# Performance work log

Measured on AMD Instinct MI355X. Metric: run time of the kernel, lower is better.

Reference implementation:

```python
import jax, jax.numpy as jnp
import numpy as np

N = 100_000      # nodes
F_IN = 512       # input feature dim
HID = 8          # hidden per head (layer 1)
HEADS = 8        # heads layer 1
CLS = 7          # num classes (layer 2 out, 1 head)
E = 1_600_000    # random edges (self-loops added in reference)
NEG_SLOPE = 0.2  # PyG GATConv default leaky_relu slope


def setup_inputs() -> dict:
    key = jax.random.key(0)
    ks = jax.random.split(key, 10)
    s1 = 1.0 / np.sqrt(F_IN)
    s2 = 1.0 / np.sqrt(HID * HEADS)
    return {
        "x": jax.random.normal(ks[0], (N, F_IN), jnp.float32),
        "edge_index": jax.random.randint(ks[1], (2, E), 0, N, dtype=jnp.int32),
        "W1": jax.random.normal(ks[2], (F_IN, HEADS * HID), jnp.float32) * s1,
        "a_src1": jax.random.normal(ks[3], (HEADS, HID), jnp.float32) * s1,
        "a_dst1": jax.random.normal(ks[4], (HEADS, HID), jnp.float32) * s1,
        "b1": jnp.zeros((HEADS * HID,), jnp.float32),
        "W2": jax.random.normal(ks[5], (HEADS * HID, CLS), jnp.float32) * s2,
        "a_src2": jax.random.normal(ks[6], (1, CLS), jnp.float32) * s2,
        "a_dst2": jax.random.normal(ks[7], (1, CLS), jnp.float32) * s2,
        "b2": jnp.zeros((CLS,), jnp.float32),
    }


def gat_layer(x, edge_index, W, a_src, a_dst, bias, concat):
    """PyG GATConv (eval mode): linear -> per-edge LeakyReLU score -> edge-softmax over
    incoming edges per dst node -> weighted scatter-sum of src messages."""
    n = x.shape[0]
    H, C = a_src.shape
    h = (x @ W).reshape(n, H, C)                      # [N, H, C]
    src, dst = edge_index[0], edge_index[1]
    alpha_src = (h * a_src).sum(-1)                   # [N, H]
    alpha_dst = (h * a_dst).sum(-1)                   # [N, H]
    e = jax.nn.leaky_relu(alpha_src[src] + alpha_dst[dst], NEG_SLOPE)  # [E, H]
    # numerically stable segment softmax over edges grouped by dst
    m = jax.ops.segment_max(e, dst, num_segments=n)   # [N, H]
    p = jnp.exp(e - m[dst])                           # [E, H]
    denom = jax.ops.segment_sum(p, dst, num_segments=n)
    alpha = p / denom[dst]                            # [E, H]
    out = jax.ops.segment_sum(alpha[:, :, None] * h[src], dst, num_segments=n)  # [N, H, C]
    out = out.reshape(n, H * C) if concat else out.mean(axis=1)
    return out + bias


def reference(x, edge_index, W1, a_src1, a_dst1, b1, W2, a_src2, a_dst2, b2):
    # add self-loops (GATConv default add_self_loops=True)
    loops = jnp.arange(N, dtype=edge_index.dtype)
    ei = jnp.concatenate([edge_index, jnp.stack([loops, loops])], axis=1)
    h = jax.nn.elu(gat_layer(x, ei, W1, a_src1, a_dst1, b1, concat=True))
    out = gat_layer(h, ei, W2, a_src2, a_dst2, b2, concat=False)
    return jax.nn.log_softmax(out, axis=1)
```

## Files before the change

kernel.cpp:

```cpp
#include <hip/hip_runtime.h>
#include <hip/hip_bf16.h>

#define NEG_SLOPE 0.2f
#define SB 256
#define HWG 384

typedef __attribute__((ext_vector_type(8))) short bfrag;
typedef __attribute__((ext_vector_type(4))) float f32x4;
typedef unsigned short ushort_t;

__device__ __forceinline__ float lrelu(float x) {
    return x >= 0.0f ? x : NEG_SLOPE * x;
}
__device__ __forceinline__ unsigned short f2bf(float f) {
    unsigned int u = __float_as_uint(f);
    u += 0x7fffu + ((u >> 16) & 1u);
    return (unsigned short)(u >> 16);
}
__device__ __forceinline__ float bf2f(unsigned short h) {
    return __uint_as_float(((unsigned int)h) << 16);
}
__device__ __forceinline__ float u2lo(unsigned int u) {
    return __uint_as_float(u << 16);
}
__device__ __forceinline__ float u2hi(unsigned int u) {
    return __uint_as_float(u & 0xffff0000u);
}

__global__ __launch_bounds__(256) void hist_prep_kernel(
    const int* __restrict__ edst, int* __restrict__ bcnt, int E, int NB,
    const float* __restrict__ W1, ushort_t* __restrict__ Whi,
    ushort_t* __restrict__ Wlo) {
    if (blockIdx.x < 128) {
        int t = blockIdx.x * 256 + threadIdx.x;
        int k = t >> 6, c = t & 63;
        float w = W1[t];
        unsigned short hi = f2bf(w);
        float rem = w - bf2f(hi);
        int dst = (k >> 7) * 8192 + c * 128 + (k & 127);
        Whi[dst] = hi;
        Wlo[dst] = f2bf(rem);
        return;
    }
    __shared__ int hist[512];
    int tid = threadIdx.x;
    for (int i = tid; i < NB; i += 256) hist[i] = 0;
    __syncthreads();
    int wg = blockIdx.x - 128;
    int CH = (E + HWG - 1) / HWG;
    int st = wg * CH, en = min(st + CH, E);
    for (int i = st + tid; i < en; i += 256)
        atomicAdd(&hist[edst[i] >> 8], 1);
    __syncthreads();
    for (int i = tid; i < NB; i += 256)
        if (hist[i] > 0) atomicAdd(&bcnt[i], hist[i]);
}

__global__ __launch_bounds__(512) void bscan_kernel(
    const int* __restrict__ bcnt, int* __restrict__ boff, int* __restrict__ bcur,
    int* __restrict__ csr_off, int NB, int N, int E) {
    __shared__ int s[512];
    int t = threadIdx.x;
    int v = (t < NB) ? bcnt[t] : 0;
    s[t] = v;
    __syncthreads();
    for (int off = 1; off < 512; off <<= 1) {
        int tv = (t >= off) ? s[t - off] : 0;
        __syncthreads();
        s[t] += tv;
        __syncthreads();
    }
    if (t < NB) {
        int o = s[t] - v;
        boff[t] = o;
        bcur[t] = o;
    }
    if (t == 0) {
        boff[NB] = E;
        csr_off[N] = E;
    }
}

__global__ __launch_bounds__(256) void gemm_bscatter_kernel(
    const float* __restrict__ x, const ushort_t* __restrict__ Whi,
    const ushort_t* __restrict__ Wlo, ushort_t* __restrict__ h1b, int n,
    const int* __restrict__ esrc, const int* __restrict__ edst,
    int* __restrict__ bcur, int2* __restrict__ ebuf, int E, int NB,
    const float* __restrict__ a_src1, const float* __restrict__ a_dst1,
    float* __restrict__ as1, float* __restrict__ ad1) {
    __shared__ int sbuf[1536];
    const int tid = threadIdx.x;

    if (blockIdx.x < SB) {
        int* hist = sbuf;
        int* base = sbuf + 512;
        int* rank = sbuf + 1024;
        for (int i = tid; i < NB; i += 256) { hist[i] = 0; rank[i] = 0; }
        __syncthreads();
        int CH = (E + SB - 1) / SB;
        int st = blockIdx.x * CH, en = min(st + CH, E);
        for (int i = st + tid; i < en; i += 256)
            atomicAdd(&hist[edst[i] >> 8], 1);
        __syncthreads();
        for (int b = tid; b < NB; b += 256)
            if (hist[b] > 0) base[b] = atomicAdd(&bcur[b], hist[b]);
        __syncthreads();
        for (int i = st + tid; i < en; i += 256) {
            int d = edst[i], s = esrc[i];
            int b = d >> 8;
            int r = atomicAdd(&rank[b], 1);
            ebuf[base[b] + r] = make_int2(s, d);
        }
        return;
    }

    const int lane = tid & 63;
    const int wave = tid >> 6;
    const int l15 = lane & 15;
    const int lq = lane >> 4;
    const int wb = (blockIdx.x - SB) * 64 + wave * 16;

    f32x4 acc[4];
    #pragma unroll
    for (int t = 0; t < 4; t++) acc[t] = (f32x4){0.f, 0.f, 0.f, 0.f};

    const int arow = min(wb + l15, n - 1);
    const float* xr = x + (size_t)arow * 512;

    for (int p = 0; p < 4; p++) {
        const ushort_t* whp = Whi + p * 8192;
        const ushort_t* wlp = Wlo + p * 8192;
        #pragma unroll
        for (int step = 0; step < 4; step++) {
            int kloc = step * 32 + lq * 8;
            int kb = p * 128 + kloc;
            float4 v0 = *(const float4*)&xr[kb];
            float4 v1 = *(const float4*)&xr[kb + 4];
            float xf[8] = {v0.x, v0.y, v0.z, v0.w, v1.x, v1.y, v1.z, v1.w};
            bfrag ah, al;
            #pragma unroll
            for (int j = 0; j < 8; j++) {
                unsigned short hi = f2bf(xf[j]);
                float rem = xf[j] - bf2f(hi);
                ah[j] = (short)hi;
                al[j] = (short)f2bf(rem);
            }
            #pragma unroll
            for (int t = 0; t < 4; t++) {
                int nrow = t * 16 + l15;
                bfrag bh = *(const bfrag*)&whp[nrow * 128 + kloc];
                bfrag bl = *(const bfrag*)&wlp[nrow * 128 + kloc];
                acc[t] = __builtin_amdgcn_mfma_f32_16x16x32_bf16(al, bh, acc[t], 0, 0, 0);
                acc[t] = __builtin_amdgcn_mfma_f32_16x16x32_bf16(ah, bl, acc[t], 0, 0, 0);
                acc[t] = __builtin_amdgcn_mfma_f32_16x16x32_bf16(ah, bh, acc[t], 0, 0, 0);
            }
        }
    }
    #pragma unroll
    for (int t = 0; t < 4; t++) {
        #pragma unroll
        for (int reg = 0; reg < 4; reg++) {
            int grow = wb + lq * 4 + reg;
            if (grow < n) h1b[(size_t)grow * 64 + t * 16 + l15] = f2bf(acc[t][reg]);
        }
    }
    const int j7 = l15 & 7;
    const int wrow = wb + lq * 4 + (j7 & 3);
    #pragma unroll
    for (int t = 0; t < 4; t++) {
        int cidx = t * 16 + l15;
        float cs = a_src1[cidx];
        float cd = a_dst1[cidx];
        float ps0 = acc[t][0] * cs, ps1 = acc[t][1] * cs;
        float ps2 = acc[t][2] * cs, ps3 = acc[t][3] * cs;
        float pd0 = acc[t][0] * cd, pd1 = acc[t][1] * cd;
        float pd2 = acc[t][2] * cd, pd3 = acc[t][3] * cd;
        #pragma unroll
        for (int off = 1; off < 8; off <<= 1) {
            ps0 += __shfl_xor(ps0, off);
            ps1 += __shfl_xor(ps1, off);
            ps2 += __shfl_xor(ps2, off);
            ps3 += __shfl_xor(ps3, off);
            pd0 += __shfl_xor(pd0, off);
            pd1 += __shfl_xor(pd1, off);
            pd2 += __shfl_xor(pd2, off);
            pd3 += __shfl_xor(pd3, off);
        }
        int h = (t << 1) | (l15 >> 3);
        if (wrow < n) {
            if (j7 < 4) {
                float sv = j7 == 0 ? ps0 : j7 == 1 ? ps1 : j7 == 2 ? ps2 : ps3;
                as1[wrow * 8 + h] = sv;
            } else {
                float dv = j7 == 4 ? pd0 : j7 == 5 ? pd1 : j7 == 6 ? pd2 : pd3;
                ad1[wrow * 8 + h] = dv;
            }
        }
    }
}

__global__ __launch_bounds__(256) void finalize_kernel(
    const int* __restrict__ boff, const int2* __restrict__ ebuf,
    int* __restrict__ csr_off, int* __restrict__ col, int N, int NB) {
    int tid = threadIdx.x;
    int b = blockIdx.x;
    __shared__ int cnt[256];
    __shared__ int cur[256];
    __shared__ int sc[256];
    cnt[tid] = 0;
    __syncthreads();
    int st = boff[b], en = boff[b + 1];
    for (int i = st + tid; i < en; i += 256)
        atomicAdd(&cnt[ebuf[i].y & 255], 1);
    __syncthreads();
    int v = cnt[tid];
    sc[tid] = v;
    __syncthreads();
    for (int off = 1; off < 256; off <<= 1) {
        int tv = (tid >= off) ? sc[tid - off] : 0;
        __syncthreads();
        sc[tid] += tv;
        __syncthreads();
    }
    int dbase = b << 8;
    int nd = min(256, N - dbase);
    int o = st + sc[tid] - v;
    if (tid < nd) {
        csr_off[dbase + tid] = o;
        cur[tid] = o;
    }
    __syncthreads();
    for (int i = st + tid; i < en; i += 256) {
        int2 p = ebuf[i];
        int r = atomicAdd(&cur[p.y & 255], 1);
        col[r] = p.x;
    }
}

__global__ __launch_bounds__(256) void agg1_kernel(
    const int* __restrict__ csr_off, const int* __restrict__ col,
    const ushort_t* __restrict__ h1b, const float* __restrict__ as1,
    const float* __restrict__ ad1,
    const float* __restrict__ b1, const float* __restrict__ W2,
    const float* __restrict__ a_src2, const float* __restrict__ a_dst2,
    float* __restrict__ g2, float* __restrict__ ad2, int n) {
    int d = blockIdx.x * 8 + (threadIdx.x >> 5);
    if (d >= n) return;
    int c = threadIdx.x & 31;
    int hd = c >> 2;
    const ushort_t* myrow = h1b + (size_t)d * 64;
    float adh = ad1[d * 8 + hd];
    float asd = as1[d * 8 + hd];
    float p0 = __expf(lrelu(asd + adh));
    unsigned int u = *(const unsigned int*)(myrow + c * 2);
    float denom = p0;
    float acc0 = p0 * u2lo(u);
    float acc1 = p0 * u2hi(u);
    int st = csr_off[d], en = csr_off[d + 1];
    int e = st;
    for (; e + 4 <= en; e += 4) {
        int s0 = col[e], s1 = col[e + 1], s2 = col[e + 2], s3 = col[e + 3];
        const ushort_t* r0 = h1b + (size_t)s0 * 64;
        const ushort_t* r1 = h1b + (size_t)s1 * 64;
        const ushort_t* r2 = h1b + (size_t)s2 * 64;
        const ushort_t* r3 = h1b + (size_t)s3 * 64;
        float a0 = as1[s0 * 8 + hd];
        float a1 = as1[s1 * 8 + hd];
        float a2 = as1[s2 * 8 + hd];
        float a3 = as1[s3 * 8 + hd];
        unsigned int u0 = *(const unsigned int*)(r0 + c * 2);
        unsigned int u1 = *(const unsigned int*)(r1 + c * 2);
        unsigned int u2 = *(const unsigned int*)(r2 + c * 2);
        unsigned int u3 = *(const unsigned int*)(r3 + c * 2);
        float q0 = __expf(lrelu(a0 + adh));
        float q1 = __expf(lrelu(a1 + adh));
        float q2 = __expf(lrelu(a2 + adh));
        float q3 = __expf(lrelu(a3 + adh));
        denom += (q0 + q1) + (q2 + q3);
        acc0 = fmaf(q0, u2lo(u0), acc0);
        acc1 = fmaf(q0, u2hi(u0), acc1);
        acc0 = fmaf(q1, u2lo(u1), acc0);
        acc1 = fmaf(q1, u2hi(u1), acc1);
        acc0 = fmaf(q2, u2lo(u2), acc0);
        acc1 = fmaf(q2, u2hi(u2), acc1);
        acc0 = fmaf(q3, u2lo(u3), acc0);
        acc1 = fmaf(q3, u2hi(u3), acc1);
    }
    for (; e < en; ++e) {
        int s0 = col[e];
        const ushort_t* r0 = h1b + (size_t)s0 * 64;
        float a0 = as1[s0 * 8 + hd];
        unsigned int u0 = *(const unsigned int*)(r0 + c * 2);
        float q0 = __expf(lrelu(a0 + adh));
        denom += q0;
        acc0 = fmaf(q0, u2lo(u0), acc0);
        acc1 = fmaf(q0, u2hi(u0), acc1);
    }
    float v0 = acc0 / denom + b1[2 * c];
    float v1 = acc1 / denom + b1[2 * c + 1];
    float h0 = v0 > 0.f ? v0 : (__expf(v0) - 1.f);
    float h1v = v1 > 0.f ? v1 : (__expf(v1) - 1.f);
    float g[7];
    #pragma unroll
    for (int j = 0; j < 7; j++) {
        float t = fmaf(h0, W2[(2 * c) * 7 + j], h1v * W2[(2 * c + 1) * 7 + j]);
        #pragma unroll
        for (int off = 1; off < 32; off <<= 1) t += __shfl_xor(t, off);
        g[j] = t;
    }
    float sa = 0.f, da = 0.f;
    #pragma unroll
    for (int j = 0; j < 7; j++) {
        sa = fmaf(g[j], a_src2[j], sa);
        da = fmaf(g[j], a_dst2[j], da);
    }
    if (c < 7) g2[(size_t)d * 8 + c] = g[c];
    if (c == 7) g2[(size_t)d * 8 + 7] = sa;
    if (c == 8) ad2[d] = da;
}

__global__ __launch_bounds__(256) void agg2_kernel(
    const int* __restrict__ csr_off, const int* __restrict__ col,
    const float* __restrict__ ad2, const float* __restrict__ g2,
    const float* __restrict__ b2, float* __restrict__ out, int n) {
    int d = blockIdx.x * 4 + (threadIdx.x >> 6);
    if (d >= n) return;
    int lane = threadIdx.x & 63;
    int j = lane >> 3, cc = lane & 7;
    int bl = lane | 7;
    float adv = ad2[d];
    float vd = g2[(size_t)d * 8 + cc];
    float as2d = __shfl(vd, bl);
    float pd = (j == 0) ? __expf(lrelu(as2d + adv)) : 0.f;
    float denom = pd;
    float acc = pd * vd;
    int st = csr_off[d], en = csr_off[d + 1];
    for (int base = st; base < en; base += 8) {
        int eidx = base + j;
        bool valid = eidx < en;
        int s = valid ? col[eidx] : d;
        float val = g2[(size_t)s * 8 + cc];
        float as2s = __shfl(val, bl);
        float p = valid ? __expf(lrelu(as2s + adv)) : 0.f;
        denom += p;
        acc = fmaf(p, val, acc);
    }
    #pragma unroll
    for (int off = 8; off < 64; off <<= 1) {
        acc += __shfl_xor(acc, off);
        denom += __shfl_xor(denom, off);
    }
    float o = acc / denom + ((cc < 7) ? b2[cc] : 0.f);
    float m = (cc < 7) ? o : -1e30f;
    #pragma unroll
    for (int off = 1; off < 8; off <<= 1) m = fmaxf(m, __shfl_xor(m, off));
    float se = (cc < 7) ? __expf(o - m) : 0.f;
    #pragma unroll
    for (int off = 1; off < 8; off <<= 1) se += __shfl_xor(se, off);
    float lse = m + __logf(se);
    if (j == 0 && cc < 7) out[(size_t)d * 7 + cc] = o - lse;
}

extern "C" void kernel_launch(void* const* d_in, const int* in_sizes, int n_in,
                              void* d_out, int out_size, void* d_ws, size_t ws_size,
                              hipStream_t stream) {
    const float* x      = (const float*)d_in[0];
    const int*   ei     = (const int*)d_in[1];
    const float* W1     = (const float*)d_in[2];
    const float* a_src1 = (const float*)d_in[3];
    const float* a_dst1 = (const float*)d_in[4];
    const float* b1     = (const float*)d_in[5];
    const float* W2     = (const float*)d_in[6];
    const float* a_src2 = (const float*)d_in[7];
    const float* a_dst2 = (const float*)d_in[8];
    const float* b2     = (const float*)d_in[9];

    int N = in_sizes[0] / 512;
    int E = in_sizes[1] / 2;
    const int* esrc = ei;
    const int* edst = ei + E;
    int NB = (N + 255) >> 8;

    char* ws = (char*)d_ws;
    size_t off = 0;
    auto alloc = [&](size_t bytes) -> void* {
        void* p = ws + off;
        off += (bytes + 255) & ~(size_t)255;
        return p;
    };
    ushort_t* h1b  = (ushort_t*)alloc((size_t)N * 64 * 2);
    float* as1     = (float*)alloc((size_t)N * 8 * 4);
    float* ad1     = (float*)alloc((size_t)N * 8 * 4);
    float* g2      = (float*)alloc((size_t)N * 8 * 4);
    float* ad2     = (float*)alloc((size_t)N * 4);
    int*   csr_off = (int*)alloc((size_t)(N + 1) * 4);
    int*   col     = (int*)alloc((size_t)E * 4);
    int2*  ebuf    = (int2*)alloc((size_t)E * 8);
    ushort_t* Whi  = (ushort_t*)alloc(512 * 64 * 2);
    ushort_t* Wlo  = (ushort_t*)alloc(512 * 64 * 2);
    int*   bcnt    = (int*)alloc((size_t)NB * 4);
    int*   boff    = (int*)alloc((size_t)(NB + 1) * 4);
    int*   bcur    = (int*)alloc((size_t)NB * 4);

    hipMemsetAsync(bcnt, 0, (size_t)NB * 4, stream);

    int gbl = (N + 63) / 64;

    hist_prep_kernel<<<128 + HWG, 256, 0, stream>>>(edst, bcnt, E, NB, W1, Whi, Wlo);
    bscan_kernel<<<1, 512, 0, stream>>>(bcnt, boff, bcur, csr_off, NB, N, E);
    gemm_bscatter_kernel<<<SB + gbl, 256, 0, stream>>>(x, Whi, Wlo, h1b, N,
                                                       esrc, edst, bcur, ebuf, E, NB,
                                                       a_src1, a_dst1, as1, ad1);
    finalize_kernel<<<NB, 256, 0, stream>>>(boff, ebuf, csr_off, col, N, NB);
    agg1_kernel<<<(N + 7) / 8, 256, 0, stream>>>(csr_off, col, h1b, as1, ad1, b1,
                                                 W2, a_src2, a_dst2, g2, ad2, N);
    agg2_kernel<<<(N + 3) / 4, 256, 0, stream>>>(csr_off, col, ad2, g2, b2,
                                                 (float*)d_out, N);
}
```

Before: 528.0 us.

## Stage split-bf16 W1 in swizzled LDS and use 1024-thread GEMM blocks

The GEMM part of the fused gemm/bucket-scatter kernel now copies the hi/lo bf16 weight halves (128 KB total) into LDS once per block, with an XOR swizzle to avoid bank conflicts. Blocks grow to 1024 threads (16 waves), and each wave takes 16-row tiles, so one weight load serves many row tiles instead of every wave re-reading W from global or L2. The scatter blocks also run at 1024 threads and reuse the LDS buffer. The cost is 128 KB of LDS per block, which allows only one block per CU and may lower occupancy for both the GEMM and the scatter part.

```diff
diff --git a/kernel.cpp b/kernel.cpp
--- a/kernel.cpp
+++ b/kernel.cpp
@@ -81,31 +81,32 @@
     }
 }
 
-__global__ __launch_bounds__(256) void gemm_bscatter_kernel(
+__global__ __launch_bounds__(1024) void gemm_bscatter_kernel(
     const float* __restrict__ x, const ushort_t* __restrict__ Whi,
     const ushort_t* __restrict__ Wlo, ushort_t* __restrict__ h1b, int n,
     const int* __restrict__ esrc, const int* __restrict__ edst,
     int* __restrict__ bcur, int2* __restrict__ ebuf, int E, int NB,
     const float* __restrict__ a_src1, const float* __restrict__ a_dst1,
     float* __restrict__ as1, float* __restrict__ ad1) {
-    __shared__ int sbuf[1536];
+    __shared__ __align__(16) ushort_t Wh[32768];
+    __shared__ __align__(16) ushort_t Wl[32768];
     const int tid = threadIdx.x;
 
     if (blockIdx.x < SB) {
-        int* hist = sbuf;
-        int* base = sbuf + 512;
-        int* rank = sbuf + 1024;
-        for (int i = tid; i < NB; i += 256) { hist[i] = 0; rank[i] = 0; }
+        int* hist = (int*)Wh;
+        int* base = hist + 512;
+        int* rank = hist + 1024;
+        for (int i = tid; i < NB; i += 1024) { hist[i] = 0; rank[i] = 0; }
         __syncthreads();
         int CH = (E + SB - 1) / SB;
         int st = blockIdx.x * CH, en = min(st + CH, E);
-        for (int i = st + tid; i < en; i += 256)
+        for (int i = st + tid; i < en; i += 1024)
             atomicAdd(&hist[edst[i] >> 8], 1);
         __syncthreads();
-        for (int b = tid; b < NB; b += 256)
+        for (int b = tid; b < NB; b += 1024)
             if (hist[b] > 0) base[b] = atomicAdd(&bcur[b], hist[b]);
         __syncthreads();
-        for (int i = st + tid; i < en; i += 256) {
+        for (int i = st + tid; i < en; i += 1024) {
             int d = edst[i], s = esrc[i];
             int b = d >> 8;
             int r = atomicAdd(&rank[b], 1);
@@ -114,86 +115,102 @@
         return;
     }
 
+    #pragma unroll
+    for (int i = 0; i < 4; i++) {
+        int lin = (tid + i * 1024) * 8;
+        int row = (lin >> 7) & 63;
+        int swz = lin ^ ((row & 7) << 3);
+        *(bfrag*)&Wh[swz] = *(const bfrag*)&Whi[lin];
+        *(bfrag*)&Wl[swz] = *(const bfrag*)&Wlo[lin];
+    }
+    __syncthreads();
+
     const int lane = tid & 63;
     const int wave = tid >> 6;
     const int l15 = lane & 15;
     const int lq = lane >> 4;
-    const int wb = (blockIdx.x - SB) * 64 + wave * 16;
-
-    f32x4 acc[4];
-    #pragma unroll
-    for (int t = 0; t < 4; t++) acc[t] = (f32x4){0.f, 0.f, 0.f, 0.f};
-
-    const int arow = min(wb + l15, n - 1);
-    const float* xr = x + (size_t)arow * 512;
-
-    for (int p = 0; p < 4; p++) {
-        const ushort_t* whp = Whi + p * 8192;
-        const ushort_t* wlp = Wlo + p * 8192;
+    const int r7s = (l15 & 7) << 3;
+
+    const int ntiles = (n + 15) >> 4;
+    const int tstride = (gridDim.x - SB) * 16;
+
+    for (int tile = (blockIdx.x - SB) * 16 + wave; tile < ntiles; tile += tstride) {
+        const int wb = tile * 16;
+        f32x4 acc[4];
         #pragma unroll
-        for (int step = 0; step < 4; step++) {
-            int kloc = step * 32 + lq * 8;
-            int kb = p * 128 + kloc;
-            float4 v0 = *(const float4*)&xr[kb];
-            float4 v1 = *(const float4*)&xr[kb + 4];
-            float xf[8] = {v0.x, v0.y, v0.z, v0.w, v1.x, v1.y, v1.z, v1.w};
-            bfrag ah, al;
+        for (int t = 0; t < 4; t++) acc[t] = (f32x4){0.f, 0.f, 0.f, 0.f};
+
+        const int arow = min(wb + l15, n - 1);
+        const float* xr = x + (size_t)arow * 512;
+
+        #pragma unroll
+        for (int p = 0; p < 4; p++) {
             #pragma unroll
-            for (int j = 0; j < 8; j++) {
-                unsigned short hi = f2bf(xf[j]);
-                float rem = xf[j] - bf2f(hi);
-                ah[j] = (short)hi;
-                al[j] = (short)f2bf(rem);
-            }
-            #pragma unroll
-            for (int t = 0; t < 4; t++) {
-                int nrow = t * 16 + l15;
-                bfrag bh = *(const bfrag*)&whp[nrow * 128 + kloc];
-                bfrag bl = *(const bfrag*)&wlp[nrow * 128 + kloc];
-                acc[t] = __builtin_amdgcn_mfma_f32_16x16x32_bf16(al, bh, acc[t], 0, 0, 0);
-                acc[t] = __builtin_amdgcn_mfma_f32_16x16x32_bf16(ah, bl, acc[t], 0, 0, 0);
-                acc[t] = __builtin_amdgcn_mfma_f32_16x16x32_bf16(ah, bh, acc[t], 0, 0, 0);
+            for (int step = 0; step < 4; step++) {
+                int kloc = step * 32 + lq * 8;
+                int kb = p * 128 + kloc;
+                float4 v0 = *(const float4*)&xr[kb];
+                float4 v1 = *(const float4*)&xr[kb + 4];
+                float xf[8] = {v0.x, v0.y, v0.z, v0.w, v1.x, v1.y, v1.z, v1.w};
+                bfrag ah, al;
+                #pragma unroll
+                for (int j = 0; j < 8; j++) {
+                    unsigned short hi = f2bf(xf[j]);
+                    float rem = xf[j] - bf2f(hi);
+                    ah[j] = (short)hi;
+                    al[j] = (short)f2bf(rem);
+                }
+                #pragma unroll
+                for (int t = 0; t < 4; t++) {
+                    int nrow = t * 16 + l15;
+                    int bidx = ((p * 64 + nrow) * 128 + kloc) ^ r7s;
+                    bfrag bh = *(const bfrag*)&Wh[bidx];
+                    bfrag bl = *(const bfrag*)&Wl[bidx];
+                    acc[t] = __builtin_amdgcn_mfma_f32_16x16x32_bf16(al, bh, acc[t], 0, 0, 0);
+                    acc[t] = __builtin_amdgcn_mfma_f32_16x16x32_bf16(ah, bl, acc[t], 0, 0, 0);
+                    acc[t] = __builtin_amdgcn_mfma_f32_16x16x32_bf16(ah, bh, acc[t], 0, 0, 0);
+                }
             }
         }
-    }
-    #pragma unroll
-    for (int t = 0; t < 4; t++) {
         #pragma unroll
-        for (int reg = 0; reg < 4; reg++) {
-            int grow = wb + lq * 4 + reg;
-            if (grow < n) h1b[(size_t)grow * 64 + t * 16 + l15] = f2bf(acc[t][reg]);
+        for (int t = 0; t < 4; t++) {
+            #pragma unroll
+            for (int reg = 0; reg < 4; reg++) {
+                int grow = wb + lq * 4 + reg;
+                if (grow < n) h1b[(size_t)grow * 64 + t * 16 + l15] = f2bf(acc[t][reg]);
+            }
         }
-    }
-    const int j7 = l15 & 7;
-    const int wrow = wb + lq * 4 + (j7 & 3);
-    #pragma unroll
-    for (int t = 0; t < 4; t++) {
-        int cidx = t * 16 + l15;
-        float cs = a_src1[cidx];
-        float cd = a_dst1[cidx];
-        float ps0 = acc[t][0] * cs, ps1 = acc[t][1] * cs;
-        float ps2 = acc[t][2] * cs, ps3 = acc[t][3] * cs;
-        float pd0 = acc[t][0] * cd, pd1 = acc[t][1] * cd;
-        float pd2 = acc[t][2] * cd, pd3 = acc[t][3] * cd;
+        const int j7 = l15 & 7;
+        const int wrow = wb + lq * 4 + (j7 & 3);
         #pragma unroll
-        for (int off = 1; off < 8; off <<= 1) {
-            ps0 += __shfl_xor(ps0, off);
-            ps1 += __shfl_xor(ps1, off);
-            ps2 += __shfl_xor(ps2, off);
-            ps3 += __shfl_xor(ps3, off);
-            pd0 += __shfl_xor(pd0, off);
-            pd1 += __shfl_xor(pd1, off);
-            pd2 += __shfl_xor(pd2, off);
-            pd3 += __shfl_xor(pd3, off);
-        }
-        int h = (t << 1) | (l15 >> 3);
-        if (wrow < n) {
-            if (j7 < 4) {
-                float sv = j7 == 0 ? ps0 : j7 == 1 ? ps1 : j7 == 2 ? ps2 : ps3;
-                as1[wrow * 8 + h] = sv;
-            } else {
-                float dv = j7 == 4 ? pd0 : j7 == 5 ? pd1 : j7 == 6 ? pd2 : pd3;
-                ad1[wrow * 8 + h] = dv;
+        for (int t = 0; t < 4; t++) {
+            int cidx = t * 16 + l15;
+            float cs = a_src1[cidx];
+            float cd = a_dst1[cidx];
+            float ps0 = acc[t][0] * cs, ps1 = acc[t][1] * cs;
+            float ps2 = acc[t][2] * cs, ps3 = acc[t][3] * cs;
+            float pd0 = acc[t][0] * cd, pd1 = acc[t][1] * cd;
+            float pd2 = acc[t][2] * cd, pd3 = acc[t][3] * cd;
+            #pragma unroll
+            for (int off = 1; off < 8; off <<= 1) {
+                ps0 += __shfl_xor(ps0, off);
+                ps1 += __shfl_xor(ps1, off);
+                ps2 += __shfl_xor(ps2, off);
+                ps3 += __shfl_xor(ps3, off);
+                pd0 += __shfl_xor(pd0, off);
+                pd1 += __shfl_xor(pd1, off);
+                pd2 += __shfl_xor(pd2, off);
+                pd3 += __shfl_xor(pd3, off);
+            }
+            int h = (t << 1) | (l15 >> 3);
+            if (wrow < n) {
+                if (j7 < 4) {
+                    float sv = j7 == 0 ? ps0 : j7 == 1 ? ps1 : j7 == 2 ? ps2 : ps3;
+                    as1[wrow * 8 + h] = sv;
+                } else {
+                    float dv = j7 == 4 ? pd0 : j7 == 5 ? pd1 : j7 == 6 ? pd2 : pd3;
+                    ad1[wrow * 8 + h] = dv;
+                }
             }
         }
     }
@@ -404,11 +421,12 @@
 
     hipMemsetAsync(bcnt, 0, (size_t)NB * 4, stream);
 
-    int gbl = (N + 63) / 64;
+    int ntiles = (N + 15) / 16;
+    int GB = (ntiles + 15) / 16;
 
     hist_prep_kernel<<<128 + HWG, 256, 0, stream>>>(edst, bcnt, E, NB, W1, Whi, Wlo);
     bscan_kernel<<<1, 512, 0, stream>>>(bcnt, boff, bcur, csr_off, NB, N, E);
-    gemm_bscatter_kernel<<<SB + gbl, 256, 0, stream>>>(x, Whi, Wlo, h1b, N,
+    gemm_bscatter_kernel<<<SB + GB, 1024, 0, stream>>>(x, Whi, Wlo, h1b, N,
                                                        esrc, edst, bcur, ebuf, E, NB,
                                                        a_src1, a_dst1, as1, ad1);
     finalize_kernel<<<NB, 256, 0, stream>>>(boff, ebuf, csr_off, col, N, NB);
```

Result: slower. 844.1 us (+59.8%).
